# Kernel optimization log

Measured on AMD Instinct MI355X. Metric: run time of the kernel, lower is better.

Reference implementation:

```python
import jax, jax.numpy as jnp
import numpy as np

D = 1024      # hidden_dim
E = 8         # num_experts
F = 512       # expert_dim


def setup_inputs() -> dict:
    key = jax.random.key(0)
    ks = jax.random.split(key, 7)
    B, N = 4, 4096
    s1 = 1.0 / np.sqrt(D)
    s2 = 1.0 / np.sqrt(F)
    return {
        "x": jax.random.normal(ks[0], (B, N, D), dtype=jnp.float32),
        "W1": jax.random.uniform(ks[1], (E, D, F), jnp.float32, -s1, s1),  # per-expert first linear
        "b1": jax.random.uniform(ks[2], (E, F), jnp.float32, -s1, s1),
        "W2": jax.random.uniform(ks[3], (E, F, D), jnp.float32, -s2, s2),  # per-expert second linear
        "b2": jax.random.uniform(ks[4], (E, D), jnp.float32, -s2, s2),
        "Wr": jax.random.uniform(ks[5], (D, E), jnp.float32, -s1, s1),    # router
        "br": jax.random.uniform(ks[6], (E,), jnp.float32, -s1, s1),
    }


def reference(x, W1, b1, W2, b2, Wr, br):
    # Router: softmax over experts per token. [B,N,E]
    router_weights = jax.nn.softmax(x @ Wr + br, axis=-1)
    # All experts on all tokens (dense soft-MoE), batched as grouped GEMMs.
    h = jax.nn.gelu(jnp.einsum('bnd,edf->bnef', x, W1) + b1, approximate=False)  # [B,N,E,F]
    y = jnp.einsum('bnef,efd->bned', h, W2) + b2[None, None]                      # [B,N,E,D]
    # Softmax-weighted combine over experts.
    return jnp.einsum('bned,bne->bnd', y, router_weights)
```

## Files before the change

### kernel.cpp

```cpp
#include <hip/hip_runtime.h>
#include <hip/hip_bf16.h>
#include <math.h>

#define MTOK 16384
#define DDIM 1024
#define EEXP 8
#define FDIM 512
#define EFK  4096

typedef __attribute__((ext_vector_type(8))) short short8;
typedef __attribute__((ext_vector_type(4))) float floatx4;

__device__ __forceinline__ void gld_lds16(const void* g, void* l) {
  __builtin_amdgcn_global_load_lds((const __attribute__((address_space(1))) void*)g,
                                   (__attribute__((address_space(3))) void*)l, 16, 0, 0);
}

__device__ __forceinline__ float gelu_fast(float v) {
  const float z  = v * 0.70710678118654752f;
  const float az = fabsf(z);
  const float t  = __builtin_amdgcn_rcpf(1.f + 0.3275911f * az);
  const float poly = t * (0.254829592f +
                     t * (-0.284496736f +
                     t * (1.421413741f +
                     t * (-1.453152027f +
                     t * 1.061405429f))));
  const float ex = __expf(-az * az);
  float erfv = 1.f - poly * ex;
  erfv = copysignf(erfv, z);
  return 0.5f * v * (1.f + erfv);
}

__global__ __launch_bounds__(256) void transpose_cast_kernel(
    const float* __restrict__ in, __hip_bfloat16* __restrict__ out, int R, int C) {
  __shared__ float tile[32][33];
  const float* inb = in + (size_t)blockIdx.z * R * C;
  __hip_bfloat16* outb = out + (size_t)blockIdx.z * R * C;
  const int c0 = blockIdx.x * 32, r0 = blockIdx.y * 32;
  const int tx = threadIdx.x & 31, ty = threadIdx.x >> 5;
#pragma unroll
  for (int i = 0; i < 4; ++i)
    tile[ty + i * 8][tx] = inb[(size_t)(r0 + ty + i * 8) * C + (c0 + tx)];
  __syncthreads();
#pragma unroll
  for (int i = 0; i < 4; ++i)
    outb[(size_t)(c0 + ty + i * 8) * R + (r0 + tx)] = __float2bfloat16(tile[tx][ty + i * 8]);
}

__global__ __launch_bounds__(256) void router_cast_kernel(
    const float* __restrict__ x, const float* __restrict__ Wr, const float* __restrict__ br,
    __hip_bfloat16* __restrict__ xbf, float* __restrict__ r) {
  const int wave = (blockIdx.x * 256 + threadIdx.x) >> 6;
  const int lane = threadIdx.x & 63;
  const float* xr = x + (size_t)wave * DDIM;
  float acc[EEXP];
#pragma unroll
  for (int e = 0; e < EEXP; ++e) acc[e] = 0.f;
#pragma unroll
  for (int i = 0; i < DDIM / 64; ++i) {
    const int d = i * 64 + lane;
    const float xv = xr[d];
    xbf[(size_t)wave * DDIM + d] = __float2bfloat16(xv);
    const float4* w4 = (const float4*)(Wr + (size_t)d * EEXP);
    const float4 w0 = w4[0], w1 = w4[1];
    acc[0] += xv * w0.x; acc[1] += xv * w0.y; acc[2] += xv * w0.z; acc[3] += xv * w0.w;
    acc[4] += xv * w1.x; acc[5] += xv * w1.y; acc[6] += xv * w1.z; acc[7] += xv * w1.w;
  }
#pragma unroll
  for (int off = 32; off; off >>= 1) {
#pragma unroll
    for (int e = 0; e < EEXP; ++e) acc[e] += __shfl_xor(acc[e], off, 64);
  }
  float mx = -1e30f;
#pragma unroll
  for (int e = 0; e < EEXP; ++e) { acc[e] += br[e]; mx = fmaxf(mx, acc[e]); }
  float s = 0.f;
#pragma unroll
  for (int e = 0; e < EEXP; ++e) { acc[e] = expf(acc[e] - mx); s += acc[e]; }
  const float inv = 1.f / s;
  if (lane < EEXP) r[(size_t)wave * EEXP + lane] = acc[lane] * inv;
}


#define TILE_A_ELEMS (128 * 32)
#define TILE_ELEMS   ((128 + 256) * 32)

__global__ __launch_bounds__(512, 4) void gemm_h_kernel(
    const __hip_bfloat16* __restrict__ A, const __hip_bfloat16* __restrict__ W1t,
    const float* __restrict__ b1, const float* __restrict__ r,
    __hip_bfloat16* __restrict__ Hs) {
  const int M0 = blockIdx.x * 128;
  const int F0 = blockIdx.y * 256;
  const int e  = blockIdx.z;

  __shared__ __hip_bfloat16 lds[2][TILE_ELEMS];

  const int tid  = threadIdx.x;
  const int lane = tid & 63;
  const int wid  = tid >> 6;
  const int fg = (wid >> 1) * 64;
  const int tg = (wid & 1) * 64;
  const int laneq = lane >> 4;
  const int lanem = lane & 15;
  const int srow = tid >> 2;
  const int cc8  = (tid & 3) * 8;

  const __hip_bfloat16* gA = A + (size_t)(M0 + srow) * DDIM + cc8;
  const __hip_bfloat16* gB = W1t + (size_t)e * FDIM * DDIM + (size_t)(F0 + srow) * DDIM + cc8;
  const __hip_bfloat16* gB2 = gB + (size_t)128 * DDIM;

  floatx4 acc[4][4];
#pragma unroll
  for (int i = 0; i < 4; ++i)
#pragma unroll
    for (int j = 0; j < 4; ++j) acc[i][j] = (floatx4){0.f, 0.f, 0.f, 0.f};

#define STAGEH(p, k0)                                               \
  do {                                                              \
    gld_lds16(gA  + (k0), &lds[p][(size_t)tid * 8]);                \
    gld_lds16(gB  + (k0), &lds[p][(size_t)(512 + tid) * 8]);        \
    gld_lds16(gB2 + (k0), &lds[p][(size_t)(1024 + tid) * 8]);       \
  } while (0)

  STAGEH(0, 0);
  const int KT = DDIM / 32;
  for (int kt = 0; kt < KT; ++kt) {
    const int p = kt & 1;
    __syncthreads();
    if (kt + 1 < KT) STAGEH(p ^ 1, (kt + 1) * 32);
    short8 wfr[4], xfr[4];
#pragma unroll
    for (int i = 0; i < 4; ++i)
      wfr[i] = *(const short8*)(&lds[p][TILE_A_ELEMS + (fg + i * 16 + lanem) * 32 + laneq * 8]);
#pragma unroll
    for (int j = 0; j < 4; ++j)
      xfr[j] = *(const short8*)(&lds[p][(tg + j * 16 + lanem) * 32 + laneq * 8]);
#pragma unroll
    for (int i = 0; i < 4; ++i)
#pragma unroll
      for (int j = 0; j < 4; ++j)
        acc[i][j] = __builtin_amdgcn_mfma_f32_16x16x32_bf16(wfr[i], xfr[j], acc[i][j], 0, 0, 0);
  }
#undef STAGEH

#pragma unroll
  for (int j = 0; j < 4; ++j) {
    const int tok = M0 + tg + j * 16 + lanem;
    const float rv = r[(size_t)tok * EEXP + e];
#pragma unroll
    for (int i = 0; i < 4; ++i) {
      const int f = F0 + fg + i * 16 + laneq * 4;
      const float4 b4 = *(const float4*)(b1 + e * FDIM + f);
      union { ushort4 u; __hip_bfloat16 h[4]; } pk;
      pk.h[0] = __float2bfloat16(gelu_fast(acc[i][j][0] + b4.x) * rv);
      pk.h[1] = __float2bfloat16(gelu_fast(acc[i][j][1] + b4.y) * rv);
      pk.h[2] = __float2bfloat16(gelu_fast(acc[i][j][2] + b4.z) * rv);
      pk.h[3] = __float2bfloat16(gelu_fast(acc[i][j][3] + b4.w) * rv);
      *(ushort4*)(Hs + (size_t)tok * EFK + e * FDIM + f) = pk.u;
    }
  }
}

__global__ __launch_bounds__(512, 4) void gemm_out_kernel(
    const __hip_bfloat16* __restrict__ Hs, const __hip_bfloat16* __restrict__ W2t,
    const float* __restrict__ b2, const float* __restrict__ r,
    float* __restrict__ out) {
  const int M0 = (blockIdx.x >> 2) * 128;
  const int N0 = (blockIdx.x & 3) * 256;

  __shared__ __hip_bfloat16 lds[2][TILE_ELEMS];

  const int tid  = threadIdx.x;
  const int lane = tid & 63;
  const int wid  = tid >> 6;
  const int dg = (wid >> 1) * 64;
  const int tg = (wid & 1) * 64;
  const int laneq = lane >> 4;
  const int lanem = lane & 15;
  const int srow = tid >> 2;
  const int cc8  = (tid & 3) * 8;

  const __hip_bfloat16* gA = Hs + (size_t)(M0 + srow) * EFK + cc8;
  const __hip_bfloat16* gB = W2t + (size_t)(N0 + srow) * EFK + cc8;
  const __hip_bfloat16* gB2 = gB + (size_t)128 * EFK;

  floatx4 acc[4][4];
#pragma unroll
  for (int i = 0; i < 4; ++i)
#pragma unroll
    for (int j = 0; j < 4; ++j) acc[i][j] = (floatx4){0.f, 0.f, 0.f, 0.f};

#define STAGEO(p, k0)                                               \
  do {                                                              \
    gld_lds16(gA  + (k0), &lds[p][(size_t)tid * 8]);                \
    gld_lds16(gB  + (k0), &lds[p][(size_t)(512 + tid) * 8]);        \
    gld_lds16(gB2 + (k0), &lds[p][(size_t)(1024 + tid) * 8]);       \
  } while (0)

  STAGEO(0, 0);
  const int KT = EFK / 32;
  for (int kt = 0; kt < KT; ++kt) {
    const int p = kt & 1;
    __syncthreads();
    if (kt + 1 < KT) STAGEO(p ^ 1, (kt + 1) * 32);
    short8 wfr[4], hfr[4];
#pragma unroll
    for (int i = 0; i < 4; ++i)
      wfr[i] = *(const short8*)(&lds[p][TILE_A_ELEMS + (dg + i * 16 + lanem) * 32 + laneq * 8]);
#pragma unroll
    for (int j = 0; j < 4; ++j)
      hfr[j] = *(const short8*)(&lds[p][(tg + j * 16 + lanem) * 32 + laneq * 8]);
#pragma unroll
    for (int i = 0; i < 4; ++i)
#pragma unroll
      for (int j = 0; j < 4; ++j)
        acc[i][j] = __builtin_amdgcn_mfma_f32_16x16x32_bf16(wfr[i], hfr[j], acc[i][j], 0, 0, 0);
  }
#undef STAGEO

#pragma unroll
  for (int i = 0; i < 4; ++i) {
    const int d0 = N0 + dg + i * 16 + laneq * 4;
    float4 b2v[EEXP];
#pragma unroll
    for (int e = 0; e < EEXP; ++e) b2v[e] = *(const float4*)(b2 + e * DDIM + d0);
#pragma unroll
    for (int j = 0; j < 4; ++j) {
      const int tok = M0 + tg + j * 16 + lanem;
      const float4* r4 = (const float4*)(r + (size_t)tok * EEXP);
      const float4 r0 = r4[0], r1 = r4[1];
      const float rv[EEXP] = {r0.x, r0.y, r0.z, r0.w, r1.x, r1.y, r1.z, r1.w};
      float bx = 0.f, by = 0.f, bz = 0.f, bw = 0.f;
#pragma unroll
      for (int e = 0; e < EEXP; ++e) {
        bx += rv[e] * b2v[e].x; by += rv[e] * b2v[e].y;
        bz += rv[e] * b2v[e].z; bw += rv[e] * b2v[e].w;
      }
      float4 o;
      o.x = acc[i][j][0] + bx; o.y = acc[i][j][1] + by;
      o.z = acc[i][j][2] + bz; o.w = acc[i][j][3] + bw;
      *(float4*)(out + (size_t)tok * DDIM + d0) = o;
    }
  }
}

extern "C" void kernel_launch(void* const* d_in, const int* in_sizes, int n_in,
                              void* d_out, int out_size, void* d_ws, size_t ws_size,
                              hipStream_t stream) {
  const float* x  = (const float*)d_in[0];
  const float* W1 = (const float*)d_in[1];
  const float* b1 = (const float*)d_in[2];
  const float* W2 = (const float*)d_in[3];
  const float* b2 = (const float*)d_in[4];
  const float* Wr = (const float*)d_in[5];
  const float* br = (const float*)d_in[6];
  float* out = (float*)d_out;

  char* ws = (char*)d_ws;
  __hip_bfloat16* xbf = (__hip_bfloat16*)(ws);
  __hip_bfloat16* W1t = (__hip_bfloat16*)(ws + (32u << 20));
  __hip_bfloat16* W2t = (__hip_bfloat16*)(ws + (40u << 20));
  float*          r   = (float*)(ws + (48u << 20));
  __hip_bfloat16* Hs  = (__hip_bfloat16*)(ws + (48u << 20) + (1u << 19));

  transpose_cast_kernel<<<dim3(FDIM / 32, DDIM / 32, EEXP), 256, 0, stream>>>(W1, W1t, DDIM, FDIM);
  transpose_cast_kernel<<<dim3(DDIM / 32, EFK / 32, 1), 256, 0, stream>>>(W2, W2t, EFK, DDIM);
  router_cast_kernel<<<MTOK / 4, 256, 0, stream>>>(x, Wr, br, xbf, r);
  gemm_h_kernel<<<dim3(MTOK / 128, FDIM / 256, EEXP), 512, 0, stream>>>(xbf, W1t, b1, r, Hs);
  gemm_out_kernel<<<dim3((MTOK / 128) * (DDIM / 256)), 512, 0, stream>>>(Hs, W2t, b2, r, out);
}
```

Before: 522.9 us.

## Rewrite both GEMMs with 256x256 tiles, K=64 swizzled LDS, and quadrant-phased pipeline

Both bf16 GEMM kernels move from 128x256 tiles with K=32 double buffering to 256x256 tiles with K=64 stages. Each stage is split into four quadrant phases that interleave global-to-LDS loads with MFMA work, using explicit vmcnt waits, barriers and s_setprio. LDS rows are XOR-swizzled to avoid bank conflicts, and block indices are remapped for better L2 locality. The aim is more reuse per loaded byte and better overlap of memory with compute. In exchange it uses more registers and 128KB of LDS per block, which lowers occupancy to 2 blocks.

```diff
diff --git a/kernel.cpp b/kernel.cpp
--- a/kernel.cpp
+++ b/kernel.cpp
@@ -81,152 +81,166 @@
   if (lane < EEXP) r[(size_t)wave * EEXP + lane] = acc[lane] * inv;
 }
 
-
-#define TILE_A_ELEMS (128 * 32)
-#define TILE_ELEMS   ((128 + 256) * 32)
-
-__global__ __launch_bounds__(512, 4) void gemm_h_kernel(
+#define BUFSZ 65536
+#define AOFF  0
+#define BOFF  32768
+
+#define STAGE_A(Q1, QM, K0)                                                        \
+  do {                                                                             \
+    _Pragma("unroll") for (int r_ = 0; r_ < 2; ++r_) {                             \
+      gld_lds16(gA + (size_t)(r_ * 128 + (QM) * 64 + wid * 8 + l3) * LDA_ +        \
+                    (K0) + ((l7 ^ l3) * 8),                                        \
+                ldsb + (Q1) * BUFSZ + AOFF + (QM) * 16384 +                        \
+                    (r_ * 64 + wid * 8) * 128);                                    \
+    }                                                                              \
+  } while (0)
+
+#define STAGE_B(Q1, QN, K0)                                                        \
+  do {                                                                             \
+    _Pragma("unroll") for (int r_ = 0; r_ < 2; ++r_) {                             \
+      const int lin_ = r_ * 64 + wid * 8 + l3;                                     \
+      gld_lds16(gB + (size_t)((lin_ >> 5) * 64 + (QN) * 32 + (lin_ & 31)) * LDB_ + \
+                    (K0) + ((l7 ^ l3) * 8),                                        \
+                ldsb + (Q1) * BUFSZ + BOFF + (QN) * 16384 +                        \
+                    (r_ * 64 + wid * 8) * 128);                                    \
+    }                                                                              \
+  } while (0)
+
+#define PHASE(P, QM, QN, VM, LA, LB, STAGE_STMT)                                   \
+  do {                                                                             \
+    asm volatile("s_waitcnt vmcnt(" VM ")\n\ts_barrier" ::: "memory");             \
+    if (LA) {                                                                      \
+      _Pragma("unroll") for (int i_ = 0; i_ < 4; ++i_)                             \
+        _Pragma("unroll") for (int k_ = 0; k_ < 2; ++k_)                           \
+          af[i_][k_] = *(const short8*)(ldsb + (P) * BUFSZ + AOFF +                \
+              (QM) * 16384 + (wr * 64 + i_ * 16 + lanem) * 128 +                   \
+              (((k_ * 4 + laneq) ^ swz) * 16));                                    \
+    }                                                                              \
+    if (LB) {                                                                      \
+      _Pragma("unroll") for (int j_ = 0; j_ < 2; ++j_)                             \
+        _Pragma("unroll") for (int k_ = 0; k_ < 2; ++k_)                           \
+          bf[j_][k_] = *(const short8*)(ldsb + (P) * BUFSZ + BOFF +                \
+              (QN) * 16384 + (wc * 32 + j_ * 16 + lanem) * 128 +                   \
+              (((k_ * 4 + laneq) ^ swz) * 16));                                    \
+    }                                                                              \
+    STAGE_STMT;                                                                    \
+    __builtin_amdgcn_s_setprio(1);                                                 \
+    _Pragma("unroll") for (int i_ = 0; i_ < 4; ++i_)                               \
+      _Pragma("unroll") for (int j_ = 0; j_ < 2; ++j_)                             \
+        _Pragma("unroll") for (int k_ = 0; k_ < 2; ++k_)                           \
+          acc[(QM) * 4 + i_][(QN) * 2 + j_] =                                      \
+              __builtin_amdgcn_mfma_f32_16x16x32_bf16(                             \
+                  af[i_][k_], bf[j_][k_], acc[(QM) * 4 + i_][(QN) * 2 + j_],       \
+                  0, 0, 0);                                                        \
+    __builtin_amdgcn_s_setprio(0);                                                 \
+  } while (0)
+
+#define GEMM_CORE(NT)                                                              \
+  STAGE_A(0, 0, 0);                                                                \
+  STAGE_B(0, 0, 0);                                                                \
+  STAGE_B(0, 1, 0);                                                                \
+  STAGE_A(0, 1, 0);                                                                \
+  for (int kt = 0; kt < (NT) - 1; ++kt) {                                          \
+    const int p_ = kt & 1, q_ = p_ ^ 1, k1_ = (kt + 1) * 64;                       \
+    PHASE(p_, 0, 0, "4", 1, 1, STAGE_A(q_, 0, k1_));                               \
+    PHASE(p_, 0, 1, "4", 0, 1, STAGE_B(q_, 0, k1_));                               \
+    PHASE(p_, 1, 1, "4", 1, 0, STAGE_B(q_, 1, k1_));                               \
+    PHASE(p_, 1, 0, "6", 0, 1, STAGE_A(q_, 1, k1_));                               \
+  }                                                                                \
+  {                                                                                \
+    const int p_ = ((NT) - 1) & 1;                                                 \
+    PHASE(p_, 0, 0, "4", 1, 1, (void)0);                                           \
+    PHASE(p_, 0, 1, "2", 0, 1, (void)0);                                           \
+    PHASE(p_, 1, 1, "0", 1, 0, (void)0);                                           \
+    PHASE(p_, 1, 0, "0", 0, 1, (void)0);                                           \
+  }
+
+__global__ __launch_bounds__(512, 2) void gemm_h_kernel(
     const __hip_bfloat16* __restrict__ A, const __hip_bfloat16* __restrict__ W1t,
     const float* __restrict__ b1, const float* __restrict__ r,
     __hip_bfloat16* __restrict__ Hs) {
-  const int M0 = blockIdx.x * 128;
-  const int F0 = blockIdx.y * 256;
-  const int e  = blockIdx.z;
-
-  __shared__ __hip_bfloat16 lds[2][TILE_ELEMS];
-
-  const int tid  = threadIdx.x;
-  const int lane = tid & 63;
-  const int wid  = tid >> 6;
-  const int fg = (wid >> 1) * 64;
-  const int tg = (wid & 1) * 64;
-  const int laneq = lane >> 4;
-  const int lanem = lane & 15;
-  const int srow = tid >> 2;
-  const int cc8  = (tid & 3) * 8;
-
-  const __hip_bfloat16* gA = A + (size_t)(M0 + srow) * DDIM + cc8;
-  const __hip_bfloat16* gB = W1t + (size_t)e * FDIM * DDIM + (size_t)(F0 + srow) * DDIM + cc8;
-  const __hip_bfloat16* gB2 = gB + (size_t)128 * DDIM;
-
-  floatx4 acc[4][4];
-#pragma unroll
-  for (int i = 0; i < 4; ++i)
+  const int bid = blockIdx.x;
+  const int strip = bid & 63, fb = (bid >> 6) & 1, e = bid >> 7;
+  const int T0 = strip * 256, F0 = fb * 256;
+
+  __shared__ char ldsb[2 * BUFSZ];
+
+  const int tid = threadIdx.x, lane = tid & 63, wid = tid >> 6;
+  const int wr = wid >> 2, wc = wid & 3;
+  const int lanem = lane & 15, laneq = lane >> 4;
+  const int l3 = lane >> 3, l7 = lane & 7;
+  const int swz = lanem & 7;
+  const int LDA_ = DDIM, LDB_ = DDIM;
+
+  const __hip_bfloat16* gA = W1t + (size_t)e * FDIM * DDIM + (size_t)F0 * DDIM;
+  const __hip_bfloat16* gB = A + (size_t)T0 * DDIM;
+
+  floatx4 acc[8][4];
+#pragma unroll
+  for (int i = 0; i < 8; ++i)
 #pragma unroll
     for (int j = 0; j < 4; ++j) acc[i][j] = (floatx4){0.f, 0.f, 0.f, 0.f};
-
-#define STAGEH(p, k0)                                               \
-  do {                                                              \
-    gld_lds16(gA  + (k0), &lds[p][(size_t)tid * 8]);                \
-    gld_lds16(gB  + (k0), &lds[p][(size_t)(512 + tid) * 8]);        \
-    gld_lds16(gB2 + (k0), &lds[p][(size_t)(1024 + tid) * 8]);       \
-  } while (0)
-
-  STAGEH(0, 0);
-  const int KT = DDIM / 32;
-  for (int kt = 0; kt < KT; ++kt) {
-    const int p = kt & 1;
-    __syncthreads();
-    if (kt + 1 < KT) STAGEH(p ^ 1, (kt + 1) * 32);
-    short8 wfr[4], xfr[4];
-#pragma unroll
-    for (int i = 0; i < 4; ++i)
-      wfr[i] = *(const short8*)(&lds[p][TILE_A_ELEMS + (fg + i * 16 + lanem) * 32 + laneq * 8]);
-#pragma unroll
-    for (int j = 0; j < 4; ++j)
-      xfr[j] = *(const short8*)(&lds[p][(tg + j * 16 + lanem) * 32 + laneq * 8]);
-#pragma unroll
-    for (int i = 0; i < 4; ++i)
-#pragma unroll
-      for (int j = 0; j < 4; ++j)
-        acc[i][j] = __builtin_amdgcn_mfma_f32_16x16x32_bf16(wfr[i], xfr[j], acc[i][j], 0, 0, 0);
-  }
-#undef STAGEH
-
-#pragma unroll
-  for (int j = 0; j < 4; ++j) {
-    const int tok = M0 + tg + j * 16 + lanem;
+  short8 af[4][2], bf[2][2];
+
+  GEMM_CORE(DDIM / 64);
+
+#pragma unroll
+  for (int nj = 0; nj < 4; ++nj) {
+    const int tok = T0 + wc * 64 + nj * 16 + lanem;
     const float rv = r[(size_t)tok * EEXP + e];
 #pragma unroll
-    for (int i = 0; i < 4; ++i) {
-      const int f = F0 + fg + i * 16 + laneq * 4;
+    for (int mi = 0; mi < 8; ++mi) {
+      const int f = F0 + wr * 128 + mi * 16 + laneq * 4;
       const float4 b4 = *(const float4*)(b1 + e * FDIM + f);
       union { ushort4 u; __hip_bfloat16 h[4]; } pk;
-      pk.h[0] = __float2bfloat16(gelu_fast(acc[i][j][0] + b4.x) * rv);
-      pk.h[1] = __float2bfloat16(gelu_fast(acc[i][j][1] + b4.y) * rv);
-      pk.h[2] = __float2bfloat16(gelu_fast(acc[i][j][2] + b4.z) * rv);
-      pk.h[3] = __float2bfloat16(gelu_fast(acc[i][j][3] + b4.w) * rv);
+      pk.h[0] = __float2bfloat16(gelu_fast(acc[mi][nj][0] + b4.x) * rv);
+      pk.h[1] = __float2bfloat16(gelu_fast(acc[mi][nj][1] + b4.y) * rv);
+      pk.h[2] = __float2bfloat16(gelu_fast(acc[mi][nj][2] + b4.z) * rv);
+      pk.h[3] = __float2bfloat16(gelu_fast(acc[mi][nj][3] + b4.w) * rv);
       *(ushort4*)(Hs + (size_t)tok * EFK + e * FDIM + f) = pk.u;
     }
   }
 }
 
-__global__ __launch_bounds__(512, 4) void gemm_out_kernel(
+__global__ __launch_bounds__(512, 2) void gemm_out_kernel(
     const __hip_bfloat16* __restrict__ Hs, const __hip_bfloat16* __restrict__ W2t,
     const float* __restrict__ b2, const float* __restrict__ r,
     float* __restrict__ out) {
-  const int M0 = (blockIdx.x >> 2) * 128;
-  const int N0 = (blockIdx.x & 3) * 256;
-
-  __shared__ __hip_bfloat16 lds[2][TILE_ELEMS];
-
-  const int tid  = threadIdx.x;
-  const int lane = tid & 63;
-  const int wid  = tid >> 6;
-  const int dg = (wid >> 1) * 64;
-  const int tg = (wid & 1) * 64;
-  const int laneq = lane >> 4;
-  const int lanem = lane & 15;
-  const int srow = tid >> 2;
-  const int cc8  = (tid & 3) * 8;
-
-  const __hip_bfloat16* gA = Hs + (size_t)(M0 + srow) * EFK + cc8;
-  const __hip_bfloat16* gB = W2t + (size_t)(N0 + srow) * EFK + cc8;
-  const __hip_bfloat16* gB2 = gB + (size_t)128 * EFK;
-
-  floatx4 acc[4][4];
-#pragma unroll
-  for (int i = 0; i < 4; ++i)
+  const int bid = blockIdx.x;
+  const int strip = (bid >> 5) * 8 + (bid & 7);
+  const int dq = (bid >> 3) & 3;
+  const int T0 = strip * 256, D0 = dq * 256;
+
+  __shared__ char ldsb[2 * BUFSZ];
+
+  const int tid = threadIdx.x, lane = tid & 63, wid = tid >> 6;
+  const int wr = wid >> 2, wc = wid & 3;
+  const int lanem = lane & 15, laneq = lane >> 4;
+  const int l3 = lane >> 3, l7 = lane & 7;
+  const int swz = lanem & 7;
+  const int LDA_ = EFK, LDB_ = EFK;
+
+  const __hip_bfloat16* gA = W2t + (size_t)D0 * EFK;
+  const __hip_bfloat16* gB = Hs + (size_t)T0 * EFK;
+
+  floatx4 acc[8][4];
+#pragma unroll
+  for (int i = 0; i < 8; ++i)
 #pragma unroll
     for (int j = 0; j < 4; ++j) acc[i][j] = (floatx4){0.f, 0.f, 0.f, 0.f};
-
-#define STAGEO(p, k0)                                               \
-  do {                                                              \
-    gld_lds16(gA  + (k0), &lds[p][(size_t)tid * 8]);                \
-    gld_lds16(gB  + (k0), &lds[p][(size_t)(512 + tid) * 8]);        \
-    gld_lds16(gB2 + (k0), &lds[p][(size_t)(1024 + tid) * 8]);       \
-  } while (0)
-
-  STAGEO(0, 0);
-  const int KT = EFK / 32;
-  for (int kt = 0; kt < KT; ++kt) {
-    const int p = kt & 1;
-    __syncthreads();
-    if (kt + 1 < KT) STAGEO(p ^ 1, (kt + 1) * 32);
-    short8 wfr[4], hfr[4];
-#pragma unroll
-    for (int i = 0; i < 4; ++i)
-      wfr[i] = *(const short8*)(&lds[p][TILE_A_ELEMS + (dg + i * 16 + lanem) * 32 + laneq * 8]);
-#pragma unroll
-    for (int j = 0; j < 4; ++j)
-      hfr[j] = *(const short8*)(&lds[p][(tg + j * 16 + lanem) * 32 + laneq * 8]);
-#pragma unroll
-    for (int i = 0; i < 4; ++i)
-#pragma unroll
-      for (int j = 0; j < 4; ++j)
-        acc[i][j] = __builtin_amdgcn_mfma_f32_16x16x32_bf16(wfr[i], hfr[j], acc[i][j], 0, 0, 0);
-  }
-#undef STAGEO
-
-#pragma unroll
-  for (int i = 0; i < 4; ++i) {
-    const int d0 = N0 + dg + i * 16 + laneq * 4;
+  short8 af[4][2], bf[2][2];
+
+  GEMM_CORE(EFK / 64);
+
+#pragma unroll
+  for (int mi = 0; mi < 8; ++mi) {
+    const int d0 = D0 + wr * 128 + mi * 16 + laneq * 4;
     float4 b2v[EEXP];
 #pragma unroll
     for (int e = 0; e < EEXP; ++e) b2v[e] = *(const float4*)(b2 + e * DDIM + d0);
 #pragma unroll
-    for (int j = 0; j < 4; ++j) {
-      const int tok = M0 + tg + j * 16 + lanem;
+    for (int nj = 0; nj < 4; ++nj) {
+      const int tok = T0 + wc * 64 + nj * 16 + lanem;
       const float4* r4 = (const float4*)(r + (size_t)tok * EEXP);
       const float4 r0 = r4[0], r1 = r4[1];
       const float rv[EEXP] = {r0.x, r0.y, r0.z, r0.w, r1.x, r1.y, r1.z, r1.w};
@@ -237,8 +251,8 @@
         bz += rv[e] * b2v[e].z; bw += rv[e] * b2v[e].w;
       }
       float4 o;
-      o.x = acc[i][j][0] + bx; o.y = acc[i][j][1] + by;
-      o.z = acc[i][j][2] + bz; o.w = acc[i][j][3] + bw;
+      o.x = acc[mi][nj][0] + bx; o.y = acc[mi][nj][1] + by;
+      o.z = acc[mi][nj][2] + bz; o.w = acc[mi][nj][3] + bw;
       *(float4*)(out + (size_t)tok * DDIM + d0) = o;
     }
   }
@@ -266,6 +280,6 @@
   transpose_cast_kernel<<<dim3(FDIM / 32, DDIM / 32, EEXP), 256, 0, stream>>>(W1, W1t, DDIM, FDIM);
   transpose_cast_kernel<<<dim3(DDIM / 32, EFK / 32, 1), 256, 0, stream>>>(W2, W2t, EFK, DDIM);
   router_cast_kernel<<<MTOK / 4, 256, 0, stream>>>(x, Wr, br, xbf, r);
-  gemm_h_kernel<<<dim3(MTOK / 128, FDIM / 256, EEXP), 512, 0, stream>>>(xbf, W1t, b1, r, Hs);
-  gemm_out_kernel<<<dim3((MTOK / 128) * (DDIM / 256)), 512, 0, stream>>>(Hs, W2t, b2, r, out);
-}
+  gemm_h_kernel<<<dim3((MTOK / 256) * (FDIM / 256) * EEXP), 512, 0, stream>>>(xbf, W1t, b1, r, Hs);
+  gemm_out_kernel<<<dim3((MTOK / 256) * (DDIM / 256)), 512, 0, stream>>>(Hs, W2t, b2, r, out);
+}
```

Result: faster. 480.8 us (-8.1%).
